# Kernel tuning notes

Measured on AMD Instinct MI355X. Metric: run time of the kernel, lower is better.

Reference implementation:

```python
import jax, jax.numpy as jnp
import numpy as np

N_GRAPHS = 256

def gcn_conv(x, src, dst, W, b, n_nodes):
    # PyG GCNConv: add self-loops, symmetric normalization, then aggregate x_j*norm at dst.
    loop = jnp.arange(n_nodes, dtype=src.dtype)
    row = jnp.concatenate([src, loop])
    col = jnp.concatenate([dst, loop])
    h = x @ W  # [N, out]
    deg = jax.ops.segment_sum(jnp.ones_like(col, dtype=h.dtype), col, num_segments=n_nodes)
    dinv = jnp.where(deg > 0, jax.lax.rsqrt(deg), 0.0)
    norm = dinv[row] * dinv[col]  # [E+N]
    msg = h[row] * norm[:, None]
    out = jax.ops.segment_sum(msg, col, num_segments=n_nodes)
    return out + b

def global_mean_pool(x, batch, num_graphs):
    s = jax.ops.segment_sum(x, batch, num_segments=num_graphs)
    cnt = jax.ops.segment_sum(jnp.ones((x.shape[0],), dtype=x.dtype), batch, num_segments=num_graphs)
    return s / jnp.maximum(cnt, 1.0)[:, None]

def setup_inputs() -> dict:
    key = jax.random.key(0)
    ks = jax.random.split(key, 9)
    N, E, F, H = 100000, 3200000, 136, 50
    x = jax.random.normal(ks[0], (N, F), dtype=jnp.float32)
    edge_index = jax.random.randint(ks[1], (2, E), 0, N, dtype=jnp.int64)
    batch = jnp.sort(jax.random.randint(ks[2], (N,), 0, N_GRAPHS, dtype=jnp.int64))
    s1 = 1.0 / np.sqrt(F)
    s2 = 1.0 / np.sqrt(H)
    W1 = jax.random.uniform(ks[3], (F, H), jnp.float32, -s1, s1)
    b1 = jnp.zeros((H,), jnp.float32)
    W2 = jax.random.uniform(ks[4], (H, H), jnp.float32, -s2, s2)
    b2 = jnp.zeros((H,), jnp.float32)
    Wl = jax.random.uniform(ks[5], (H, 1), jnp.float32, -s2, s2)
    bl = jnp.zeros((1,), jnp.float32)
    return {"x": x, "edge_index": edge_index, "batch": batch,
            "W1": W1, "b1": b1, "W2": W2, "b2": b2, "Wl": Wl, "bl": bl}

def reference(x, edge_index, batch, W1, b1, W2, b2, Wl, bl):
    n = x.shape[0]
    src, dst = edge_index[0], edge_index[1]
    h = jax.nn.relu(gcn_conv(x, src, dst, W1, b1, n))
    h = jax.nn.relu(gcn_conv(h, src, dst, W2, b2, n))
    g = global_mean_pool(h, batch, N_GRAPHS)
    # Dropout is inference-identity (deterministic baseline).
    out = jax.nn.sigmoid(g @ Wl + bl)
    return out.flatten()
```

## Files before the change

### kernel.cpp

```cpp
#include <hip/hip_runtime.h>
#include <math.h>

#define HH 50
#define BSH 8
#define BSZ 256
#define CH 8192
#define SCH 4096

typedef float floatx2 __attribute__((ext_vector_type(2)));

__device__ __forceinline__ unsigned int f2bf_pair(float f0, float f1) {
    unsigned int u0 = __float_as_uint(f0);
    unsigned int u1 = __float_as_uint(f1);
    u0 = (u0 + 0x7FFFu + ((u0 >> 16) & 1u)) >> 16;
    u1 = (u1 + 0x7FFFu + ((u1 >> 16) & 1u)) >> 16;
    return u0 | (u1 << 16);
}
__device__ __forceinline__ float bf_lo(unsigned int p) { return __uint_as_float(p << 16); }
__device__ __forceinline__ float bf_hi(unsigned int p) { return __uint_as_float(p & 0xFFFF0000u); }

__device__ __forceinline__ unsigned int pack4_fp8(float f0, float f1, float f2, float f3) {
    int r = 0;
    r = __builtin_amdgcn_cvt_pk_fp8_f32(f0, f1, r, false);
    r = __builtin_amdgcn_cvt_pk_fp8_f32(f2, f3, r, true);
    return (unsigned int)r;
}

__global__ void histA_kernel(const int* __restrict__ ei, int E, int NB, int NC,
                             int* __restrict__ blockHist) {
    __shared__ int hist[512];
    int c = blockIdx.x;
    int tid = threadIdx.x;
    for (int i = tid; i < 512; i += 256) hist[i] = 0;
    __syncthreads();
    int beg = c * CH, end = min(E, beg + CH);
    for (int i = beg + tid; i < end; i += 256) {
        int d = ei[(size_t)E + i];
        atomicAdd(&hist[d >> BSH], 1);
    }
    __syncthreads();
    for (int i = tid; i < NB; i += 256) blockHist[i * NC + c] = hist[i];
}

__global__ void scan1_kernel(const int* __restrict__ bh, int M, int* __restrict__ csum) {
    __shared__ int red[4];
    int tid = threadIdx.x;
    int lane = tid & 63, wv = tid >> 6;
    int base = blockIdx.x * SCH + tid * 16;
    int s = 0;
    if (base + 16 <= M) {
#pragma unroll
        for (int j = 0; j < 4; j++) {
            int4 v = *(const int4*)(bh + base + 4 * j);
            s += v.x + v.y + v.z + v.w;
        }
    } else {
        for (int j = 0; j < 16 && base + j < M; j++) s += bh[base + j];
    }
    for (int off = 1; off < 64; off <<= 1) s += __shfl_xor(s, off);
    if (lane == 0) red[wv] = s;
    __syncthreads();
    if (tid == 0) csum[blockIdx.x] = red[0] + red[1] + red[2] + red[3];
}

__global__ void scan2_kernel(int* __restrict__ csum, int nb,
                             int* __restrict__ rowptr, int N, int E) {
    int lane = threadIdx.x;
    int v = (lane < nb) ? csum[lane] : 0;
    int orig = v;
    for (int off = 1; off < 64; off <<= 1) {
        int u = __shfl_up(v, off);
        if (lane >= off) v += u;
    }
    if (lane < nb) csum[lane] = v - orig;
    if (lane == 0) rowptr[N] = E;
}

__global__ void scan3_kernel(const int* __restrict__ bh, int M, const int* __restrict__ csum,
                             int* __restrict__ scanned) {
    __shared__ int wsum[4];
    int tid = threadIdx.x;
    int lane = tid & 63, wv = tid >> 6;
    int base = blockIdx.x * SCH + tid * 16;
    int a[16];
#pragma unroll
    for (int j = 0; j < 16; j++) a[j] = 0;
    if (base + 16 <= M) {
#pragma unroll
        for (int j = 0; j < 4; j++) {
            int4 v = *(const int4*)(bh + base + 4 * j);
            a[4 * j] = v.x; a[4 * j + 1] = v.y; a[4 * j + 2] = v.z; a[4 * j + 3] = v.w;
        }
    } else {
        for (int j = 0; j < 16 && base + j < M; j++) a[j] = bh[base + j];
    }
    int t = 0;
#pragma unroll
    for (int j = 0; j < 16; j++) t += a[j];
    int inc = t;
    for (int off = 1; off < 64; off <<= 1) {
        int u = __shfl_up(inc, off);
        if (lane >= off) inc += u;
    }
    if (lane == 63) wsum[wv] = inc;
    __syncthreads();
    int wb = 0;
    for (int w = 0; w < wv; w++) wb += wsum[w];
    int run = csum[blockIdx.x] + wb + (inc - t);
    if (base + 16 <= M) {
#pragma unroll
        for (int j = 0; j < 4; j++) {
            int4 o;
            o.x = run; run += a[4 * j];
            o.y = run; run += a[4 * j + 1];
            o.z = run; run += a[4 * j + 2];
            o.w = run; run += a[4 * j + 3];
            *(int4*)(scanned + base + 4 * j) = o;
        }
    } else {
        for (int j = 0; j < 16 && base + j < M; j++) { scanned[base + j] = run; run += a[j]; }
    }
}

__global__ void scatterB_kernel(const int* __restrict__ ei, int E, int NB, int NC,
                                const int* __restrict__ scanned, int* __restrict__ ebuf) {
    __shared__ int offs[512];
    int c = blockIdx.x;
    int tid = threadIdx.x;
    for (int i = tid; i < NB; i += 512) offs[i] = scanned[i * NC + c];
    __syncthreads();
    int beg = c * CH, end = min(E, beg + CH);
    for (int i = beg + tid; i < end; i += 512) {
        int s = ei[i];
        int d = ei[(size_t)E + i];
        int b = d >> BSH;
        int pos = atomicAdd(&offs[b], 1);
        ebuf[pos] = ((d & (BSZ - 1)) << 17) | s;
    }
}

__global__ void buildC_kernel(const int* __restrict__ ebuf, const int* __restrict__ scanned,
                              int NB, int NC, int N, int E,
                              int* __restrict__ rowptr, float* __restrict__ dinv,
                              int* __restrict__ colidx) {
    __shared__ int cnt[BSZ], woff[BSZ], part[BSZ];
    int b = blockIdx.x;
    int tid = threadIdx.x;
    int ebeg = scanned[b * NC];
    int eend = (b == NB - 1) ? E : scanned[(b + 1) * NC];
    if (tid < BSZ) cnt[tid] = 0;
    __syncthreads();
    for (int i = ebeg + tid; i < eend; i += 512) {
        atomicAdd(&cnt[ebuf[i] >> 17], 1);
    }
    __syncthreads();
    if (tid < BSZ) part[tid] = cnt[tid];
    __syncthreads();
    for (int off = 1; off < BSZ; off <<= 1) {
        int v = 0;
        if (tid < BSZ && tid >= off) v = part[tid - off];
        __syncthreads();
        if (tid < BSZ) part[tid] += v;
        __syncthreads();
    }
    if (tid < BSZ) {
        int ex = (tid == 0) ? 0 : part[tid - 1];
        woff[tid] = ex;
        int node = (b << BSH) + tid;
        if (node < N) {
            rowptr[node] = ebeg + ex;
            dinv[node] = 1.0f / sqrtf((float)(cnt[tid] + 1));
        }
    }
    __syncthreads();
    for (int i = ebeg + tid; i < eend; i += 512) {
        int p = ebuf[i];
        int dl = p >> 17;
        int s = p & 0x1FFFF;
        int pos = atomicAdd(&woff[dl], 1);
        colidx[ebeg + pos] = s;
    }
}

__global__ void gemm_f32_kernel(const float* __restrict__ in, int K, int f4stride,
                                const float* __restrict__ W, int H,
                                const float* __restrict__ dinv,
                                unsigned int* __restrict__ hsA,
                                unsigned int* __restrict__ hsB, int N) {
    __shared__ float xs[8][128];
    __shared__ float ws[8][64];
    int tid = threadIdx.x;
    int row0 = blockIdx.x * 128;
    int rg = tid >> 3;
    int cg = tid & 7;
    int rl = tid >> 1;
    int h  = tid & 1;
    int ks = h * 4;
    float acc[4][8];
#pragma unroll
    for (int r = 0; r < 4; r++)
#pragma unroll
        for (int c = 0; c < 8; c++) acc[r][c] = 0.0f;
    const float4* inf4 = (const float4*)in;
    int rowA = row0 + rl;

    for (int k0 = 0; k0 < K; k0 += 8) {
        for (int i = tid; i < 512; i += 256) {
            int k = i >> 6, c = i & 63;
            ws[k][c] = (k0 + k < K && c < H) ? W[(k0 + k) * H + c] : 0.0f;
        }
        {
            float4 xv = make_float4(0.f, 0.f, 0.f, 0.f);
            if (rowA < N) xv = inf4[(size_t)rowA * f4stride + (k0 >> 2) + h];
            xs[ks + 0][rl] = xv.x; xs[ks + 1][rl] = xv.y;
            xs[ks + 2][rl] = xv.z; xs[ks + 3][rl] = xv.w;
        }
        __syncthreads();
#pragma unroll
        for (int k = 0; k < 8; k++) {
            float4 xa = *(const float4*)&xs[k][rg * 4];
            float4 wa = *(const float4*)&ws[k][cg * 8];
            float4 wb = *(const float4*)&ws[k][cg * 8 + 4];
            float xr[4] = {xa.x, xa.y, xa.z, xa.w};
            float wc[8] = {wa.x, wa.y, wa.z, wa.w, wb.x, wb.y, wb.z, wb.w};
#pragma unroll
            for (int r = 0; r < 4; r++)
#pragma unroll
                for (int c = 0; c < 8; c++) acc[r][c] += xr[r] * wc[c];
        }
        __syncthreads();
    }
#pragma unroll
    for (int r = 0; r < 4; r++) {
        int row = row0 + rg * 4 + r;
        if (row < N) {
            float dv = dinv[row];
            uint2 o;
            o.x = pack4_fp8(acc[r][0] * dv, acc[r][1] * dv, acc[r][2] * dv, acc[r][3] * dv);
            o.y = pack4_fp8(acc[r][4] * dv, acc[r][5] * dv, acc[r][6] * dv, acc[r][7] * dv);
            if (cg < 4) ((uint2*)(hsA + (size_t)row * 8))[cg] = o;
            else        ((uint2*)(hsB + (size_t)row * 8))[cg - 4] = o;
        }
    }
}

__global__ void gemm_bf16_kernel(const unsigned int* __restrict__ in, int K,
                                 const float* __restrict__ W, int H,
                                 const float* __restrict__ dinv,
                                 unsigned int* __restrict__ hsA,
                                 unsigned int* __restrict__ hsB, int N) {
    __shared__ float xs[8][128];
    __shared__ float ws[8][64];
    int tid = threadIdx.x;
    int row0 = blockIdx.x * 128;
    int rg = tid >> 3;
    int cg = tid & 7;
    int rl = tid >> 1;
    int h  = tid & 1;
    int ks = h * 4;
    float acc[4][8];
#pragma unroll
    for (int r = 0; r < 4; r++)
#pragma unroll
        for (int c = 0; c < 8; c++) acc[r][c] = 0.0f;
    const uint2* inu2 = (const uint2*)in;
    int rowA = row0 + rl;

    for (int k0 = 0; k0 < K; k0 += 8) {
        for (int i = tid; i < 512; i += 256) {
            int k = i >> 6, c = i & 63;
            ws[k][c] = (k0 + k < K && c < H) ? W[(k0 + k) * H + c] : 0.0f;
        }
        {
            uint2 xv = make_uint2(0u, 0u);
            if (rowA < N) xv = inu2[(size_t)rowA * 16 + (k0 >> 2) + h];
            xs[ks + 0][rl] = bf_lo(xv.x); xs[ks + 1][rl] = bf_hi(xv.x);
            xs[ks + 2][rl] = bf_lo(xv.y); xs[ks + 3][rl] = bf_hi(xv.y);
        }
        __syncthreads();
#pragma unroll
        for (int k = 0; k < 8; k++) {
            float4 xa = *(const float4*)&xs[k][rg * 4];
            float4 wa = *(const float4*)&ws[k][cg * 8];
            float4 wb = *(const float4*)&ws[k][cg * 8 + 4];
            float xr[4] = {xa.x, xa.y, xa.z, xa.w};
            float wc[8] = {wa.x, wa.y, wa.z, wa.w, wb.x, wb.y, wb.z, wb.w};
#pragma unroll
            for (int r = 0; r < 4; r++)
#pragma unroll
                for (int c = 0; c < 8; c++) acc[r][c] += xr[r] * wc[c];
        }
        __syncthreads();
    }
#pragma unroll
    for (int r = 0; r < 4; r++) {
        int row = row0 + rg * 4 + r;
        if (row < N) {
            float dv = dinv[row];
            uint2 o;
            o.x = pack4_fp8(acc[r][0] * dv, acc[r][1] * dv, acc[r][2] * dv, acc[r][3] * dv);
            o.y = pack4_fp8(acc[r][4] * dv, acc[r][5] * dv, acc[r][6] * dv, acc[r][7] * dv);
            if (cg < 4) ((uint2*)(hsA + (size_t)row * 8))[cg] = o;
            else        ((uint2*)(hsB + (size_t)row * 8))[cg - 4] = o;
        }
    }
}

__global__ void agg_half_kernel(const unsigned int* __restrict__ hsh,
                                const int* __restrict__ rowptr, const int* __restrict__ colidx,
                                const float* __restrict__ dinv, const float* __restrict__ bias,
                                int cbase, unsigned int* __restrict__ outbuf, int N) {
    int t = blockIdx.x * blockDim.x + threadIdx.x;
    int node = t >> 3;
    int q = t & 7;
    if (node >= N) return;
    const unsigned int* basq = hsh + q;
    unsigned int sv = basq[(size_t)node * 8];
    floatx2 plo = __builtin_amdgcn_cvt_pk_f32_fp8((int)sv, false);
    floatx2 phi = __builtin_amdgcn_cvt_pk_f32_fp8((int)sv, true);
    float a0 = plo[0], a1 = plo[1], a2 = phi[0], a3 = phi[1];
    int beg = rowptr[node], end = rowptr[node + 1];
    int e = beg;
    for (; e + 4 <= end; e += 4) {
        int s0 = colidx[e], s1 = colidx[e + 1], s2 = colidx[e + 2], s3 = colidx[e + 3];
        unsigned int v0 = basq[(size_t)s0 * 8];
        unsigned int v1 = basq[(size_t)s1 * 8];
        unsigned int v2 = basq[(size_t)s2 * 8];
        unsigned int v3 = basq[(size_t)s3 * 8];
        floatx2 l0 = __builtin_amdgcn_cvt_pk_f32_fp8((int)v0, false);
        floatx2 h0 = __builtin_amdgcn_cvt_pk_f32_fp8((int)v0, true);
        floatx2 l1 = __builtin_amdgcn_cvt_pk_f32_fp8((int)v1, false);
        floatx2 h1 = __builtin_amdgcn_cvt_pk_f32_fp8((int)v1, true);
        floatx2 l2 = __builtin_amdgcn_cvt_pk_f32_fp8((int)v2, false);
        floatx2 h2 = __builtin_amdgcn_cvt_pk_f32_fp8((int)v2, true);
        floatx2 l3 = __builtin_amdgcn_cvt_pk_f32_fp8((int)v3, false);
        floatx2 h3 = __builtin_amdgcn_cvt_pk_f32_fp8((int)v3, true);
        a0 += (l0[0] + l1[0]) + (l2[0] + l3[0]);
        a1 += (l0[1] + l1[1]) + (l2[1] + l3[1]);
        a2 += (h0[0] + h1[0]) + (h2[0] + h3[0]);
        a3 += (h0[1] + h1[1]) + (h2[1] + h3[1]);
    }
    for (; e < end; e++) {
        int s0 = colidx[e];
        unsigned int v0 = basq[(size_t)s0 * 8];
        floatx2 l0 = __builtin_amdgcn_cvt_pk_f32_fp8((int)v0, false);
        floatx2 h0 = __builtin_amdgcn_cvt_pk_f32_fp8((int)v0, true);
        a0 += l0[0]; a1 += l0[1]; a2 += h0[0]; a3 += h0[1];
    }
    float dv = dinv[node];
    int c0 = cbase + q * 4;
    float b0 = (c0 + 0 < HH) ? bias[c0 + 0] : 0.0f;
    float b1 = (c0 + 1 < HH) ? bias[c0 + 1] : 0.0f;
    float b2 = (c0 + 2 < HH) ? bias[c0 + 2] : 0.0f;
    float b3 = (c0 + 3 < HH) ? bias[c0 + 3] : 0.0f;
    float r0 = fmaxf(a0 * dv + b0, 0.0f);
    float r1 = fmaxf(a1 * dv + b1, 0.0f);
    float r2 = fmaxf(a2 * dv + b2, 0.0f);
    float r3 = fmaxf(a3 * dv + b3, 0.0f);
    uint2 w;
    if (c0 >= HH) { w.x = 0u; w.y = 0u; }
    else { w.x = f2bf_pair(r0, r1); w.y = f2bf_pair(r2, r3); }
    ((uint2*)outbuf)[(size_t)node * 16 + (cbase >> 2) + q] = w;
}

__global__ void pool_head_kernel(const unsigned int* __restrict__ h,
                                 const int* __restrict__ batch, int N,
                                 const float* __restrict__ Wl, const float* __restrict__ bl,
                                 float* __restrict__ out, int G) {
    __shared__ float4 red[16][16];
    int b = blockIdx.x;
    int t = threadIdx.x;
    int sub = t >> 4, q = t & 15;
    int beg, end;
    {
        int lo = 0, hi = N;
        while (lo < hi) { int mid = (lo + hi) >> 1; if (batch[mid] < b) lo = mid + 1; else hi = mid; }
        beg = lo;
        lo = 0; hi = N;
        while (lo < hi) { int mid = (lo + hi) >> 1; if (batch[mid] < b + 1) lo = mid + 1; else hi = mid; }
        end = lo;
    }
    const uint2* base = (const uint2*)h;
    float4 acc = make_float4(0.f, 0.f, 0.f, 0.f);
    for (int node = beg + sub; node < end; node += 16) {
        uint2 v = base[(size_t)node * 16 + q];
        acc.x += bf_lo(v.x); acc.y += bf_hi(v.x); acc.z += bf_lo(v.y); acc.w += bf_hi(v.y);
    }
    red[sub][q] = acc;
    __syncthreads();
#pragma unroll
    for (int off = 8; off >= 1; off >>= 1) {
        if (sub < off) {
            float4 a = red[sub][q], c = red[sub + off][q];
            a.x += c.x; a.y += c.y; a.z += c.z; a.w += c.w;
            red[sub][q] = a;
        }
        __syncthreads();
    }
    if (t == 0) {
        const float* g = (const float*)&red[0][0];
        float dot = 0.0f;
        for (int c = 0; c < HH; c++) dot += g[c] * Wl[c];
        float cnt = (float)(end - beg);
        float x = dot / fmaxf(cnt, 1.0f) + bl[0];
        out[b] = 1.0f / (1.0f + expf(-x));
    }
}

extern "C" void kernel_launch(void* const* d_in, const int* in_sizes, int n_in,
                              void* d_out, int out_size, void* d_ws, size_t ws_size,
                              hipStream_t stream) {
    const float* x     = (const float*)d_in[0];
    const int*   ei    = (const int*)d_in[1];
    const int*   batch = (const int*)d_in[2];
    const float* W1    = (const float*)d_in[3];
    const float* b1    = (const float*)d_in[4];
    const float* W2    = (const float*)d_in[5];
    const float* b2    = (const float*)d_in[6];
    const float* Wl    = (const float*)d_in[7];
    const float* bl    = (const float*)d_in[8];
    float* out = (float*)d_out;

    int N = in_sizes[2];
    int E = in_sizes[1] / 2;
    int F = in_sizes[0] / N;
    int G = out_size;

    int NB = (N + BSZ - 1) >> BSH;
    int NC = (E + CH - 1) / CH;
    int M  = NB * NC;
    int NS = (M + SCH - 1) / SCH;

    char* ws = (char*)d_ws;
    size_t off = 0;
    auto alloc = [&](size_t bytes) -> void* {
        void* p = ws + off;
        off += (bytes + 255) & ~(size_t)255;
        return p;
    };
    size_t halfBytes = (size_t)N * 32;
    size_t bufBytes  = (size_t)N * 128;
    size_t ebufBytes = (size_t)E * 4;
    float*        dinv      = (float*)alloc((size_t)N * 4);
    int*          rowptr    = (int*)alloc((size_t)(N + 1) * 4);
    int*          colidx    = (int*)alloc(ebufBytes);
    unsigned int* hsA       = (unsigned int*)alloc(halfBytes);
    unsigned int* hsB       = (unsigned int*)alloc(halfBytes);
    unsigned int* buf       = (unsigned int*)alloc(bufBytes > ebufBytes ? bufBytes : ebufBytes);
    int*          blockHist = (int*)alloc((size_t)M * 4);
    int*          scanned   = (int*)alloc((size_t)M * 4);
    int*          csum      = (int*)alloc((size_t)NS * 4 + 256);
    int*          ebuf      = (int*)buf;

    histA_kernel<<<NC, 256, 0, stream>>>(ei, E, NB, NC, blockHist);
    scan1_kernel<<<NS, 256, 0, stream>>>(blockHist, M, csum);
    scan2_kernel<<<1, 64, 0, stream>>>(csum, NS, rowptr, N, E);
    scan3_kernel<<<NS, 256, 0, stream>>>(blockHist, M, csum, scanned);
    scatterB_kernel<<<NC, 512, 0, stream>>>(ei, E, NB, NC, scanned, ebuf);
    buildC_kernel<<<NB, 512, 0, stream>>>(ebuf, scanned, NB, NC, N, E, rowptr, dinv, colidx);

    int aggBlocks = ((N * 8) + 255) / 256;
    int gemmBlocks = (N + 127) / 128;

    gemm_f32_kernel<<<gemmBlocks, 256, 0, stream>>>(x, F, F / 4, W1, HH, dinv, hsA, hsB, N);
    agg_half_kernel<<<aggBlocks, 256, 0, stream>>>(hsA, rowptr, colidx, dinv, b1, 0,  buf, N);
    agg_half_kernel<<<aggBlocks, 256, 0, stream>>>(hsB, rowptr, colidx, dinv, b1, 32, buf, N);

    gemm_bf16_kernel<<<gemmBlocks, 256, 0, stream>>>(buf, 50, W2, HH, dinv, hsA, hsB, N);
    agg_half_kernel<<<aggBlocks, 256, 0, stream>>>(hsA, rowptr, colidx, dinv, b2, 0,  buf, N);
    agg_half_kernel<<<aggBlocks, 256, 0, stream>>>(hsB, rowptr, colidx, dinv, b2, 32, buf, N);

    pool_head_kernel<<<G, 256, 0, stream>>>(buf, batch, N, Wl, bl, out, G);
}
```

Baseline: 256.5 us.

## Stage scatter in shared memory for coalesced writes; deepen GEMM K-tile to 16

The bucket scatter kernel now does a local prefix scan of its per-chunk bucket counts. It places packed edges into a shared-memory staging array first, then writes them out contiguously per bucket using a binary search over the local offsets. This replaces random global writes with mostly coalesced runs. Separately, both dense GEMM kernels now process 16 K values per tile instead of 8, halving the barrier count. The cost is more shared memory (32KB staging), which lowers occupancy, plus an extra scan and a per-element binary search.

```diff
diff --git a/kernel.cpp b/kernel.cpp
--- a/kernel.cpp
+++ b/kernel.cpp
@@ -123,19 +123,42 @@
 }
 
 __global__ void scatterB_kernel(const int* __restrict__ ei, int E, int NB, int NC,
+                                const int* __restrict__ blockHist,
                                 const int* __restrict__ scanned, int* __restrict__ ebuf) {
-    __shared__ int offs[512];
+    __shared__ int part[512];
+    __shared__ int lofs[512];
+    __shared__ int gofs[512];
+    __shared__ int cur[512];
+    __shared__ int epack[CH];
     int c = blockIdx.x;
     int tid = threadIdx.x;
-    for (int i = tid; i < NB; i += 512) offs[i] = scanned[i * NC + c];
-    __syncthreads();
-    int beg = c * CH, end = min(E, beg + CH);
+    int v = (tid < NB) ? blockHist[tid * NC + c] : 0;
+    part[tid] = v;
+    __syncthreads();
+    for (int off = 1; off < 512; off <<= 1) {
+        int u = (tid >= off) ? part[tid - off] : 0;
+        __syncthreads();
+        part[tid] += u;
+        __syncthreads();
+    }
+    int ex = (tid == 0) ? 0 : part[tid - 1];
+    lofs[tid] = ex;
+    cur[tid] = ex;
+    if (tid < NB) gofs[tid] = scanned[tid * NC + c];
+    __syncthreads();
+    int beg = c * CH, end = min(E, beg + CH), len = end - beg;
     for (int i = beg + tid; i < end; i += 512) {
         int s = ei[i];
         int d = ei[(size_t)E + i];
         int b = d >> BSH;
-        int pos = atomicAdd(&offs[b], 1);
-        ebuf[pos] = ((d & (BSZ - 1)) << 17) | s;
+        int pos = atomicAdd(&cur[b], 1);
+        epack[pos] = ((d & (BSZ - 1)) << 17) | s;
+    }
+    __syncthreads();
+    for (int j = tid; j < len; j += 512) {
+        int lo = 0, hi = NB - 1;
+        while (lo < hi) { int mid = (lo + hi + 1) >> 1; if (lofs[mid] <= j) lo = mid; else hi = mid - 1; }
+        ebuf[gofs[lo] + (j - lofs[lo])] = epack[j];
     }
 }
 
@@ -187,15 +210,14 @@
                                 const float* __restrict__ dinv,
                                 unsigned int* __restrict__ hsA,
                                 unsigned int* __restrict__ hsB, int N) {
-    __shared__ float xs[8][128];
-    __shared__ float ws[8][64];
+    __shared__ float xs[16][128];
+    __shared__ float ws[16][64];
     int tid = threadIdx.x;
     int row0 = blockIdx.x * 128;
     int rg = tid >> 3;
     int cg = tid & 7;
     int rl = tid >> 1;
     int h  = tid & 1;
-    int ks = h * 4;
     float acc[4][8];
 #pragma unroll
     for (int r = 0; r < 4; r++)
@@ -204,20 +226,28 @@
     const float4* inf4 = (const float4*)in;
     int rowA = row0 + rl;
 
-    for (int k0 = 0; k0 < K; k0 += 8) {
-        for (int i = tid; i < 512; i += 256) {
+    for (int k0 = 0; k0 < K; k0 += 16) {
+        for (int i = tid; i < 1024; i += 256) {
             int k = i >> 6, c = i & 63;
             ws[k][c] = (k0 + k < K && c < H) ? W[(k0 + k) * H + c] : 0.0f;
         }
         {
-            float4 xv = make_float4(0.f, 0.f, 0.f, 0.f);
-            if (rowA < N) xv = inf4[(size_t)rowA * f4stride + (k0 >> 2) + h];
-            xs[ks + 0][rl] = xv.x; xs[ks + 1][rl] = xv.y;
-            xs[ks + 2][rl] = xv.z; xs[ks + 3][rl] = xv.w;
-        }
-        __syncthreads();
-#pragma unroll
-        for (int k = 0; k < 8; k++) {
+            int qa = h, qb = h + 2;
+            int g1 = min((k0 >> 2) + qa, f4stride - 1);
+            int g2 = min((k0 >> 2) + qb, f4stride - 1);
+            float4 xv1 = make_float4(0.f, 0.f, 0.f, 0.f), xv2 = xv1;
+            if (rowA < N) {
+                xv1 = inf4[(size_t)rowA * f4stride + g1];
+                xv2 = inf4[(size_t)rowA * f4stride + g2];
+            }
+            xs[qa * 4 + 0][rl] = xv1.x; xs[qa * 4 + 1][rl] = xv1.y;
+            xs[qa * 4 + 2][rl] = xv1.z; xs[qa * 4 + 3][rl] = xv1.w;
+            xs[qb * 4 + 0][rl] = xv2.x; xs[qb * 4 + 1][rl] = xv2.y;
+            xs[qb * 4 + 2][rl] = xv2.z; xs[qb * 4 + 3][rl] = xv2.w;
+        }
+        __syncthreads();
+#pragma unroll
+        for (int k = 0; k < 16; k++) {
             float4 xa = *(const float4*)&xs[k][rg * 4];
             float4 wa = *(const float4*)&ws[k][cg * 8];
             float4 wb = *(const float4*)&ws[k][cg * 8 + 4];
@@ -249,15 +279,14 @@
                                  const float* __restrict__ dinv,
                                  unsigned int* __restrict__ hsA,
                                  unsigned int* __restrict__ hsB, int N) {
-    __shared__ float xs[8][128];
-    __shared__ float ws[8][64];
+    __shared__ float xs[16][128];
+    __shared__ float ws[16][64];
     int tid = threadIdx.x;
     int row0 = blockIdx.x * 128;
     int rg = tid >> 3;
     int cg = tid & 7;
     int rl = tid >> 1;
     int h  = tid & 1;
-    int ks = h * 4;
     float acc[4][8];
 #pragma unroll
     for (int r = 0; r < 4; r++)
@@ -265,21 +294,30 @@
         for (int c = 0; c < 8; c++) acc[r][c] = 0.0f;
     const uint2* inu2 = (const uint2*)in;
     int rowA = row0 + rl;
-
-    for (int k0 = 0; k0 < K; k0 += 8) {
-        for (int i = tid; i < 512; i += 256) {
+    int KP = 64;
+
+    for (int k0 = 0; k0 < KP; k0 += 16) {
+        for (int i = tid; i < 1024; i += 256) {
             int k = i >> 6, c = i & 63;
             ws[k][c] = (k0 + k < K && c < H) ? W[(k0 + k) * H + c] : 0.0f;
         }
         {
-            uint2 xv = make_uint2(0u, 0u);
-            if (rowA < N) xv = inu2[(size_t)rowA * 16 + (k0 >> 2) + h];
-            xs[ks + 0][rl] = bf_lo(xv.x); xs[ks + 1][rl] = bf_hi(xv.x);
-            xs[ks + 2][rl] = bf_lo(xv.y); xs[ks + 3][rl] = bf_hi(xv.y);
-        }
-        __syncthreads();
-#pragma unroll
-        for (int k = 0; k < 8; k++) {
+            int qa = h, qb = h + 2;
+            int g1 = (k0 >> 2) + qa;
+            int g2 = (k0 >> 2) + qb;
+            uint2 xv1 = make_uint2(0u, 0u), xv2 = xv1;
+            if (rowA < N) {
+                xv1 = inu2[(size_t)rowA * 16 + g1];
+                xv2 = inu2[(size_t)rowA * 16 + g2];
+            }
+            xs[qa * 4 + 0][rl] = bf_lo(xv1.x); xs[qa * 4 + 1][rl] = bf_hi(xv1.x);
+            xs[qa * 4 + 2][rl] = bf_lo(xv1.y); xs[qa * 4 + 3][rl] = bf_hi(xv1.y);
+            xs[qb * 4 + 0][rl] = bf_lo(xv2.x); xs[qb * 4 + 1][rl] = bf_hi(xv2.x);
+            xs[qb * 4 + 2][rl] = bf_lo(xv2.y); xs[qb * 4 + 3][rl] = bf_hi(xv2.y);
+        }
+        __syncthreads();
+#pragma unroll
+        for (int k = 0; k < 16; k++) {
             float4 xa = *(const float4*)&xs[k][rg * 4];
             float4 wa = *(const float4*)&ws[k][cg * 8];
             float4 wb = *(const float4*)&ws[k][cg * 8 + 4];
@@ -456,7 +494,7 @@
     scan1_kernel<<<NS, 256, 0, stream>>>(blockHist, M, csum);
     scan2_kernel<<<1, 64, 0, stream>>>(csum, NS, rowptr, N, E);
     scan3_kernel<<<NS, 256, 0, stream>>>(blockHist, M, csum, scanned);
-    scatterB_kernel<<<NC, 512, 0, stream>>>(ei, E, NB, NC, scanned, ebuf);
+    scatterB_kernel<<<NC, 512, 0, stream>>>(ei, E, NB, NC, blockHist, scanned, ebuf);
     buildC_kernel<<<NB, 512, 0, stream>>>(ebuf, scanned, NB, NC, N, E, rowptr, dinv, colidx);
 
     int aggBlocks = ((N * 8) + 255) / 256;
```

Result: no change. 257.7 us (+0.5%).
